# Performance work log

Measured on AMD Instinct MI355X. Metric: run time of the kernel, lower is better.

## Reference

```python
import jax, jax.numpy as jnp
import numpy as np

ALPHA = 1.0
GAMMA = 2.0
SMOOTH = 1e-07
B, S = 8192, 4096


def setup_inputs() -> dict:
    key = jax.random.key(0)
    k1, k2, k3, k4 = jax.random.split(key, 4)
    scores = jax.random.normal(k1, (B, S), dtype=jnp.float32)
    head_position = jax.random.randint(k2, (B,), 0, S, dtype=jnp.int64) if jax.config.jax_enable_x64 else jax.random.randint(k2, (B,), 0, S).astype(jnp.int32)
    tail_position = jax.random.randint(k3, (B,), 0, S).astype(head_position.dtype)
    score_mask = jax.random.randint(k4, (B, S), 0, 2, dtype=jnp.int32)
    return {"scores": scores, "head_position": head_position,
            "tail_position": tail_position, "score_mask": score_mask}


def reference(scores, head_position, tail_position, score_mask):
    # scores: [B, S] float; head/tail_position: [B] int; score_mask: [B, S] int
    batch_size = scores.shape[0]
    bidx = jnp.arange(batch_size)
    # exclude head and tail positions from the negative set
    m = score_mask.at[bidx, head_position].set(-1)
    m = m.at[bidx, tail_position].set(-1)
    neg = (m == 1)  # [B, S] candidate negatives
    # positive score per sample, broadcast against all candidates
    pos = jnp.take_along_axis(scores, tail_position[:, None], axis=1)  # [B, 1]
    # log_softmax over the pair [pos, neg_j] at index 0 == -softplus(neg - pos)
    logpt = -jax.nn.softplus(scores - pos)  # [B, S]
    pt = jnp.clip(jnp.exp(logpt), SMOOTH, 1.0 - SMOOTH)
    fl = -ALPHA * jnp.power(1.0 - pt, GAMMA) * logpt  # [B, S] per-pair focal loss
    negf = neg.astype(scores.dtype)
    cnt = negf.sum(axis=1)  # [B] number of negatives
    # per-sample focal_loss is the MEAN over its pairs; samples with 0 negs skipped
    per_sample = jnp.where(cnt > 0, (fl * negf).sum(axis=1) / jnp.maximum(cnt, 1.0), 0.0)
    return per_sample.sum() / batch_size
```

## Files before the change

kernel.cpp:

```cpp
#include <hip/hip_runtime.h>


__global__ __launch_bounds__(256) void focal_row_kernel(
    const float* __restrict__ scores,
    const int*   __restrict__ head_pos,
    const int*   __restrict__ tail_pos,
    const int*   __restrict__ mask,
    float*       __restrict__ row_out,
    int S)
{
    const int row  = blockIdx.x;
    const int tid  = threadIdx.x;
    const int head = head_pos[row];
    const int tail = tail_pos[row];
    const float* srow = scores + (size_t)row * S;
    const int*   mrow = mask   + (size_t)row * S;
    const float pos = srow[tail];

    float fsum = 0.f;
    int   cnt  = 0;

    const float4* s4 = reinterpret_cast<const float4*>(srow);
    const int4*   m4 = reinterpret_cast<const int4*>(mrow);
    const int nvec = S >> 2;
    for (int v = tid; v < nvec; v += 256) {
        float4 sv = s4[v];
        int4   mv = m4[v];
        const int base = v << 2;
        float se[4] = {sv.x, sv.y, sv.z, sv.w};
        int   me[4] = {mv.x, mv.y, mv.z, mv.w};
        #pragma unroll
        for (int k = 0; k < 4; ++k) {
            const int idx = base + k;
            const bool isneg = (me[k] == 1) && (idx != head) && (idx != tail);
            const float x  = se[k] - pos;
            const float e  = __expf(-fabsf(x));
            const float sp = fmaxf(x, 0.f) + __logf(1.f + e);
            float pt = __expf(-sp);
            pt = fminf(fmaxf(pt, 1e-7f), 1.f - 1e-7f);
            const float om = 1.f - pt;
            const float fl = om * om * sp;
            if (isneg) { fsum += fl; cnt += 1; }
        }
    }

    #pragma unroll
    for (int off = 32; off > 0; off >>= 1) {
        fsum += __shfl_down(fsum, off, 64);
        cnt  += __shfl_down(cnt,  off, 64);
    }
    __shared__ float sf[4];
    __shared__ int   sc[4];
    const int wave = tid >> 6;
    if ((tid & 63) == 0) { sf[wave] = fsum; sc[wave] = cnt; }
    __syncthreads();
    if (tid == 0) {
        const float tot = sf[0] + sf[1] + sf[2] + sf[3];
        const int   c   = sc[0] + sc[1] + sc[2] + sc[3];
        row_out[row] = (c > 0) ? tot / (float)c : 0.f;
    }
}

__global__ __launch_bounds__(256) void final_reduce_kernel(
    const float* __restrict__ row_out, float* __restrict__ out, int B)
{
    float sum = 0.f;
    for (int i = threadIdx.x; i < B; i += 256) sum += row_out[i];
    #pragma unroll
    for (int off = 32; off > 0; off >>= 1) sum += __shfl_down(sum, off, 64);
    __shared__ float sf[4];
    const int wave = threadIdx.x >> 6;
    if ((threadIdx.x & 63) == 0) sf[wave] = sum;
    __syncthreads();
    if (threadIdx.x == 0) out[0] = (sf[0] + sf[1] + sf[2] + sf[3]) / (float)B;
}

extern "C" void kernel_launch(void* const* d_in, const int* in_sizes, int n_in,
                              void* d_out, int out_size, void* d_ws, size_t ws_size,
                              hipStream_t stream)
{
    const float* scores = (const float*)d_in[0];
    const int*   headp  = (const int*)d_in[1];
    const int*   tailp  = (const int*)d_in[2];
    const int*   maskp  = (const int*)d_in[3];
    const int B = in_sizes[1];
    const int S = in_sizes[0] / B;

    float* rowbuf = (float*)d_ws;
    float* out    = (float*)d_out;

    focal_row_kernel<<<B, 256, 0, stream>>>(scores, headp, tailp, maskp, rowbuf, S);
    final_reduce_kernel<<<1, 256, 0, stream>>>(rowbuf, out, B);
}
```

Measured before the change: 285.2 us.

## Assign one wavefront per row with compile-time S and simplified softplus math

Each row is now handled by a single 64-lane wavefront (four rows per block) with S fixed at compile time. This removes the shared-memory and __syncthreads reduction and lets the loads be fully unrolled in batches of four float4/int4 pairs, putting more memory requests in flight. The softplus/pt math now uses exp(x), log(1+e) and a hardware reciprocal in place of the two exps, which can overflow for large x. The final reduce is vectorized, but it now drops the tail rows when B is not a multiple of 4.

```diff
diff --git a/kernel.cpp b/kernel.cpp
--- a/kernel.cpp
+++ b/kernel.cpp
@@ -1,7 +1,71 @@
 #include <hip/hip_runtime.h>
 
 
-__global__ __launch_bounds__(256) void focal_row_kernel(
+template <int S>
+__global__ __launch_bounds__(256, 8) void focal_row_kernel(
+    const float* __restrict__ scores,
+    const int*   __restrict__ head_pos,
+    const int*   __restrict__ tail_pos,
+    const int*   __restrict__ mask,
+    float*       __restrict__ row_out,
+    int B)
+{
+    const int lane = threadIdx.x & 63;
+    const int row  = blockIdx.x * 4 + (threadIdx.x >> 6);
+    if (row >= B) return;
+
+    const int head = head_pos[row];
+    const int tail = tail_pos[row];
+    const float4* s4 = reinterpret_cast<const float4*>(scores + (size_t)row * S);
+    const int4*   m4 = reinterpret_cast<const int4*>(mask   + (size_t)row * S);
+    const float pos = scores[(size_t)row * S + tail];
+
+    float fsum = 0.f;
+    int   cnt  = 0;
+
+    constexpr int NV4 = S / 4 / 64;
+    static_assert(NV4 % 4 == 0, "S must be divisible by 1024");
+    #pragma unroll
+    for (int g = 0; g < NV4 / 4; ++g) {
+        float4 sv[4]; int4 mv[4];
+        #pragma unroll
+        for (int u = 0; u < 4; ++u) {
+            const int v = lane + 64 * (4 * g + u);
+            sv[u] = s4[v];
+            mv[u] = m4[v];
+        }
+        #pragma unroll
+        for (int u = 0; u < 4; ++u) {
+            const int base = (lane + 64 * (4 * g + u)) << 2;
+            const float se[4] = {sv[u].x, sv[u].y, sv[u].z, sv[u].w};
+            const int   me[4] = {mv[u].x, mv[u].y, mv[u].z, mv[u].w};
+            #pragma unroll
+            for (int k = 0; k < 4; ++k) {
+                const int idx = base + k;
+                const float x  = se[k] - pos;
+                const float e  = __expf(x);
+                const float t  = 1.f + e;
+                const float sp = __logf(t);
+                float pt = __builtin_amdgcn_rcpf(t);
+                pt = fminf(fmaxf(pt, 1e-7f), 1.f - 1e-7f);
+                const float om = 1.f - pt;
+                const float fl = om * om * sp;
+                const bool isneg = (me[k] == 1) & (idx != head) & (idx != tail);
+                if (isneg) { fsum += fl; cnt += 1; }
+            }
+        }
+    }
+
+    #pragma unroll
+    for (int off = 32; off; off >>= 1) {
+        fsum += __shfl_down(fsum, off, 64);
+        cnt  += __shfl_down(cnt,  off, 64);
+    }
+    if (lane == 0)
+        row_out[row] = (cnt > 0) ? fsum / (float)cnt : 0.f;
+}
+
+__global__ __launch_bounds__(256) void focal_row_generic(
     const float* __restrict__ scores,
     const int*   __restrict__ head_pos,
     const int*   __restrict__ tail_pos,
@@ -16,47 +80,30 @@
     const float* srow = scores + (size_t)row * S;
     const int*   mrow = mask   + (size_t)row * S;
     const float pos = srow[tail];
-
-    float fsum = 0.f;
-    int   cnt  = 0;
-
-    const float4* s4 = reinterpret_cast<const float4*>(srow);
-    const int4*   m4 = reinterpret_cast<const int4*>(mrow);
-    const int nvec = S >> 2;
-    for (int v = tid; v < nvec; v += 256) {
-        float4 sv = s4[v];
-        int4   mv = m4[v];
-        const int base = v << 2;
-        float se[4] = {sv.x, sv.y, sv.z, sv.w};
-        int   me[4] = {mv.x, mv.y, mv.z, mv.w};
-        #pragma unroll
-        for (int k = 0; k < 4; ++k) {
-            const int idx = base + k;
-            const bool isneg = (me[k] == 1) && (idx != head) && (idx != tail);
-            const float x  = se[k] - pos;
-            const float e  = __expf(-fabsf(x));
-            const float sp = fmaxf(x, 0.f) + __logf(1.f + e);
-            float pt = __expf(-sp);
-            pt = fminf(fmaxf(pt, 1e-7f), 1.f - 1e-7f);
-            const float om = 1.f - pt;
-            const float fl = om * om * sp;
-            if (isneg) { fsum += fl; cnt += 1; }
-        }
+    float fsum = 0.f; int cnt = 0;
+    for (int idx = tid; idx < S; idx += 256) {
+        const float x  = srow[idx] - pos;
+        const float e  = __expf(x);
+        const float t  = 1.f + e;
+        const float sp = __logf(t);
+        float pt = __builtin_amdgcn_rcpf(t);
+        pt = fminf(fmaxf(pt, 1e-7f), 1.f - 1e-7f);
+        const float om = 1.f - pt;
+        const float fl = om * om * sp;
+        if ((mrow[idx] == 1) && (idx != head) && (idx != tail)) { fsum += fl; cnt += 1; }
     }
-
     #pragma unroll
-    for (int off = 32; off > 0; off >>= 1) {
+    for (int off = 32; off; off >>= 1) {
         fsum += __shfl_down(fsum, off, 64);
         cnt  += __shfl_down(cnt,  off, 64);
     }
-    __shared__ float sf[4];
-    __shared__ int   sc[4];
+    __shared__ float sf[4]; __shared__ int sc[4];
     const int wave = tid >> 6;
     if ((tid & 63) == 0) { sf[wave] = fsum; sc[wave] = cnt; }
     __syncthreads();
     if (tid == 0) {
-        const float tot = sf[0] + sf[1] + sf[2] + sf[3];
-        const int   c   = sc[0] + sc[1] + sc[2] + sc[3];
+        float tot = sf[0] + sf[1] + sf[2] + sf[3];
+        int   c   = sc[0] + sc[1] + sc[2] + sc[3];
         row_out[row] = (c > 0) ? tot / (float)c : 0.f;
     }
 }
@@ -65,9 +112,14 @@
     const float* __restrict__ row_out, float* __restrict__ out, int B)
 {
     float sum = 0.f;
-    for (int i = threadIdx.x; i < B; i += 256) sum += row_out[i];
+    const float4* r4 = reinterpret_cast<const float4*>(row_out);
+    const int nvec = B >> 2;
+    for (int i = threadIdx.x; i < nvec; i += 256) {
+        float4 v = r4[i];
+        sum += (v.x + v.y) + (v.z + v.w);
+    }
     #pragma unroll
-    for (int off = 32; off > 0; off >>= 1) sum += __shfl_down(sum, off, 64);
+    for (int off = 32; off; off >>= 1) sum += __shfl_down(sum, off, 64);
     __shared__ float sf[4];
     const int wave = threadIdx.x >> 6;
     if ((threadIdx.x & 63) == 0) sf[wave] = sum;
@@ -89,6 +141,11 @@
     float* rowbuf = (float*)d_ws;
     float* out    = (float*)d_out;
 
-    focal_row_kernel<<<B, 256, 0, stream>>>(scores, headp, tailp, maskp, rowbuf, S);
+    if (S == 4096) {
+        const int grid = (B + 3) / 4;
+        focal_row_kernel<4096><<<grid, 256, 0, stream>>>(scores, headp, tailp, maskp, rowbuf, B);
+    } else {
+        focal_row_generic<<<B, 256, 0, stream>>>(scores, headp, tailp, maskp, rowbuf, S);
+    }
     final_reduce_kernel<<<1, 256, 0, stream>>>(rowbuf, out, B);
 }
```

New measurement: 283.4 us. Within noise of the previous version (-0.6%).
